# Kernel optimization log

Measured on AMD Instinct MI355X. Metric: run time of the kernel, lower is better.

Reference implementation:

```python
import jax, jax.numpy as jnp
import numpy as np

HIDDEN = 1408
HEADS = 16
HEAD_DIM = 88  # HIDDEN // HEADS
NUM_PATCHES = 576  # (336 // 14) ** 2
SEQ = NUM_PATCHES + 1  # +1 CLS token position in mllama4 rope cache
ROPE_BASE = 10000.0
SCALE = HEAD_DIM ** -0.5


def _rope_cos_sin():
    # Faithful to vLLM Llama4VisionRotaryEmbedding cos/sin cache.
    idx = np.arange(NUM_PATCHES, dtype=np.int64).reshape(NUM_PATCHES, 1)
    idx = np.concatenate([idx, idx[:1]], axis=0)
    idx[-1, -1] = -2  # CLS token id -> zero rotation
    n = int(np.sqrt(NUM_PATCHES))  # patches per side = 24
    fx = idx % n
    fy = idx // n
    rd = HEAD_DIM // 2  # rotary_dim = 44
    inv = 1.0 / ROPE_BASE ** (np.arange(0, rd, 2, dtype=np.float32) / rd)  # (22,)
    # repeat_interleave(2) then cat then [::2] == concat of the two 22-d halves
    freqs = np.concatenate(
        [(fx + 1)[..., None] * inv[None, None, :], (fy + 1)[..., None] * inv[None, None, :]],
        axis=-1,
    )  # (SEQ, 1, 44)
    freqs = np.where(idx.reshape(-1, 1, 1) < 0, 0.0, freqs).astype(np.float32)
    freqs = freqs.squeeze(1)  # (SEQ, 44)
    return jnp.asarray(np.cos(freqs)), jnp.asarray(np.sin(freqs))


_COS, _SIN = _rope_cos_sin()


def _apply_rope(x, cos, sin):
    # x: [B, S, H, D]; complex rotation over adjacent pairs (is_neox_style=False)
    B, S, H, D = x.shape
    xp = x.reshape(B, S, H, D // 2, 2)
    x0, x1 = xp[..., 0], xp[..., 1]
    c = cos[None, :, None, :]  # [1, S, 1, D//2]
    s = sin[None, :, None, :]
    out = jnp.stack([x0 * c - x1 * s, x0 * s + x1 * c], axis=-1)
    return out.reshape(B, S, H, D)


def setup_inputs() -> dict:
    key = jax.random.key(0)
    k1, k2, k3, k4, k5 = jax.random.split(key, 5)
    std = HIDDEN ** -0.5
    return {
        "hidden_states": jax.random.normal(k1, (32, SEQ, HIDDEN), dtype=jnp.float32),
        "w_qkv": jax.random.normal(k2, (HIDDEN, 3 * HIDDEN), dtype=jnp.float32) * std,
        "b_qkv": jax.random.normal(k3, (3 * HIDDEN,), dtype=jnp.float32) * 0.02,
        "w_o": jax.random.normal(k4, (HIDDEN, HIDDEN), dtype=jnp.float32) * std,
        "b_o": jax.random.normal(k5, (HIDDEN,), dtype=jnp.float32) * 0.02,
    }


def reference(hidden_states, w_qkv, b_qkv, w_o, b_o):
    B, S, _ = hidden_states.shape
    qkv = hidden_states @ w_qkv + b_qkv  # [B, S, 3*HIDDEN]
    q, k, v = jnp.split(qkv, 3, axis=-1)
    q = q.reshape(B, S, HEADS, HEAD_DIM)
    k = k.reshape(B, S, HEADS, HEAD_DIM)
    v = v.reshape(B, S, HEADS, HEAD_DIM)
    q = _apply_rope(q, _COS, _SIN)
    k = _apply_rope(k, _COS, _SIN)
    scores = jnp.einsum("bqhd,bkhd->bhqk", q, k) * SCALE
    probs = jax.nn.softmax(scores, axis=-1)
    attn = jnp.einsum("bhqk,bkhd->bqhd", probs, v).reshape(B, S, HIDDEN)
    return attn @ w_o + b_o
```

## Files before the change

### kernel.cpp

```cpp
#include <hip/hip_runtime.h>
#include <math.h>

#define HEADS    16
#define HEAD_DIM 88
#define SEQ      577
#define SEQV     640
#define HIDDEN   1408
#define NQKV     4224
#define NQKV_PAD 4352
#define NOUT_PAD 1536
#define RD       44
#define SCALE_F  0.1066003581778052f
#define MPAD_ROWS 18688
#define NKT      22
#define BUF_SH   32768

typedef __attribute__((ext_vector_type(8))) short bf16x8;
typedef __attribute__((ext_vector_type(4))) float f32x4;

__device__ __forceinline__ unsigned short f2bf(float x) {
    unsigned u = __float_as_uint(x);
    unsigned r = u + 0x7fff + ((u >> 16) & 1);
    return (unsigned short)(r >> 16);
}
__device__ __forceinline__ f32x4 fzero() {
    f32x4 z; z.x = 0.f; z.y = 0.f; z.z = 0.f; z.w = 0.f; return z;
}
__device__ __forceinline__ int xcd_swz(int flat, int nwg) {
    int q = nwg >> 3, r = nwg & 7;
    int x = flat & 7, j = flat >> 3;
    return (x < r ? x * (q + 1) : r * (q + 1) + (x - r) * q) + j;
}

__global__ void rope_precompute(float* __restrict__ cosb, float* __restrict__ sinb) {
    int s = blockIdx.x;
    int j = threadIdx.x;
    if (j >= RD) return;
    float c, sn;
    if (s == SEQ - 1) {
        c = 1.f; sn = 0.f;
    } else {
        int fx = s % 24, fy = s / 24;
        int p = (j < 22) ? j : j - 22;
        float inv = powf(10000.f, -(float)p / 22.f);
        float f = (float)((j < 22 ? fx : fy) + 1) * inv;
        c = cosf(f); sn = sinf(f);
    }
    cosb[s * RD + j] = c;
    sinb[s * RD + j] = sn;
}

__global__ void conv_hs(const float* __restrict__ in, unsigned short* __restrict__ out,
                        long nreal, long ntot) {
    long i = ((long)blockIdx.x * 256 + threadIdx.x) * 4;
    if (i >= ntot) return;
    ushort4 o;
    if (i < nreal) {
        float4 v = *(const float4*)(in + i);
        o = make_ushort4(f2bf(v.x), f2bf(v.y), f2bf(v.z), f2bf(v.w));
    } else {
        o = make_ushort4(0, 0, 0, 0);
    }
    *(ushort4*)(out + i) = o;
}

__global__ void conv_wT(const float* __restrict__ in, unsigned short* __restrict__ out,
                        int R, int Creal) {
    __shared__ float t[32][33];
    int bx = blockIdx.x * 32, by = blockIdx.y * 32;
    int tx = threadIdx.x & 31, ty = threadIdx.x >> 5;
    #pragma unroll
    for (int i = 0; i < 4; ++i) {
        int col = bx + tx;
        t[ty + i * 8][tx] = (col < Creal) ? in[(size_t)(by + ty + i * 8) * Creal + col] : 0.f;
    }
    __syncthreads();
    #pragma unroll
    for (int i = 0; i < 4; ++i)
        out[(size_t)(bx + ty + i * 8) * R + by + tx] = f2bf(t[tx][ty + i * 8]);
}

__device__ __forceinline__ void stage_half(const unsigned short* __restrict__ src,
                                           int kt, unsigned short* lds, int tid) {
    #pragma unroll
    for (int q = 0; q < 2; ++q) {
        int cf = tid + 512 * q;
        int r  = cf >> 3, c = cf & 7;
        int cg = c ^ (r & 7);
        __builtin_amdgcn_global_load_lds(
            (const __attribute__((address_space(1))) void*)(src + (size_t)r * HIDDEN + kt * 64 + cg * 8),
            (__attribute__((address_space(3))) void*)(lds + cf * 8),
            16, 0, 0);
    }
}

template<int N> __device__ __forceinline__ void vwait() {
    if constexpr (N >= 0)
        asm volatile("s_waitcnt vmcnt(%0)" :: "i"(N) : "memory");
}

template<int CBUF, int IH, int JH, bool STG, int SSIDE, int SHALF, int SBUF, int WAITN>
__device__ __forceinline__ void phase8(
    const unsigned short* __restrict__ wsrc, const unsigned short* __restrict__ hsrc,
    unsigned short* smem, int skt, int tid,
    int ww, int wh, int quad, int l15, f32x4 (&acc)[8][4])
{
    bf16x8 afr[4][2], bfr[2][2];
    #pragma unroll
    for (int i2 = 0; i2 < 4; ++i2)
        #pragma unroll
        for (int kk = 0; kk < 2; ++kk) {
            int r = ww * 64 + i2 * 16 + l15;
            afr[i2][kk] = *(const bf16x8*)(smem + CBUF * BUF_SH + IH * 8192
                          + r * 64 + (((kk * 4 + quad) ^ (r & 7)) << 3));
        }
    #pragma unroll
    for (int j2 = 0; j2 < 2; ++j2)
        #pragma unroll
        for (int kk = 0; kk < 2; ++kk) {
            int r = wh * 32 + j2 * 16 + l15;
            bfr[j2][kk] = *(const bf16x8*)(smem + CBUF * BUF_SH + 16384 + JH * 8192
                          + r * 64 + (((kk * 4 + quad) ^ (r & 7)) << 3));
        }
    if constexpr (STG) {
        const unsigned short* s = (SSIDE ? hsrc : wsrc) + (size_t)SHALF * 128 * HIDDEN;
        stage_half(s, skt, smem + SBUF * BUF_SH + (SSIDE ? 16384 : 0) + SHALF * 8192, tid);
    }
    __builtin_amdgcn_sched_barrier(0);
    __builtin_amdgcn_s_barrier();
    __builtin_amdgcn_sched_barrier(0);
    __builtin_amdgcn_s_setprio(1);
    #pragma unroll
    for (int i2 = 0; i2 < 4; ++i2)
        #pragma unroll
        for (int j2 = 0; j2 < 2; ++j2)
            #pragma unroll
            for (int kk = 0; kk < 2; ++kk)
                acc[IH * 4 + i2][JH * 2 + j2] = __builtin_amdgcn_mfma_f32_16x16x32_bf16(
                    afr[i2][kk], bfr[j2][kk], acc[IH * 4 + i2][JH * 2 + j2], 0, 0, 0);
    __builtin_amdgcn_s_setprio(0);
    __builtin_amdgcn_sched_barrier(0);
    vwait<WAITN>();
    __builtin_amdgcn_s_barrier();
    __builtin_amdgcn_sched_barrier(0);
}

__device__ __forceinline__ void gemm256_8ph(
    const unsigned short* __restrict__ wsrc, const unsigned short* __restrict__ hsrc,
    unsigned short* smem, int tid, f32x4 (&acc)[8][4])
{
    const int lane = tid & 63, w8 = tid >> 6;
    const int quad = lane >> 4, l15 = lane & 15;
    const int ww = w8 >> 2, wh = w8 & 3;

    stage_half(wsrc,                0, smem,                  tid);
    stage_half(hsrc,                0, smem + 16384,          tid);
    stage_half(wsrc + 128 * HIDDEN, 0, smem + 8192,           tid);
    stage_half(hsrc + 128 * HIDDEN, 0, smem + 24576,          tid);
    stage_half(wsrc,                1, smem + BUF_SH,         tid);
    stage_half(hsrc,                1, smem + BUF_SH + 16384, tid);
    asm volatile("s_waitcnt vmcnt(4)" ::: "memory");
    __builtin_amdgcn_s_barrier();
    __builtin_amdgcn_sched_barrier(0);

    for (int it = 0; it < 10; ++it) {
        int k1 = 2 * it + 1, k2 = 2 * it + 2, k3 = 2 * it + 3;
        phase8<0,0,0, true,0,1,1,  6>(wsrc, hsrc, smem, k1, tid, ww, wh, quad, l15, acc);
        phase8<0,0,1, true,1,1,1, -1>(wsrc, hsrc, smem, k1, tid, ww, wh, quad, l15, acc);
        phase8<0,1,0, true,0,0,0, -1>(wsrc, hsrc, smem, k2, tid, ww, wh, quad, l15, acc);
        phase8<0,1,1, true,1,0,0,  8>(wsrc, hsrc, smem, k2, tid, ww, wh, quad, l15, acc);
        phase8<1,0,0, true,0,1,0,  6>(wsrc, hsrc, smem, k2, tid, ww, wh, quad, l15, acc);
        phase8<1,0,1, true,1,1,0, -1>(wsrc, hsrc, smem, k2, tid, ww, wh, quad, l15, acc);
        phase8<1,1,0, true,0,0,1, -1>(wsrc, hsrc, smem, k3, tid, ww, wh, quad, l15, acc);
        phase8<1,1,1, true,1,0,1,  8>(wsrc, hsrc, smem, k3, tid, ww, wh, quad, l15, acc);
    }
    phase8<0,0,0, true,0,1,1,  6>(wsrc, hsrc, smem, 21, tid, ww, wh, quad, l15, acc);
    phase8<0,0,1, true,1,1,1, -1>(wsrc, hsrc, smem, 21, tid, ww, wh, quad, l15, acc);
    phase8<0,1,0, false,0,0,0, -1>(wsrc, hsrc, smem, 0, tid, ww, wh, quad, l15, acc);
    phase8<0,1,1, false,0,0,0,  4>(wsrc, hsrc, smem, 0, tid, ww, wh, quad, l15, acc);
    phase8<1,0,0, false,0,0,0,  0>(wsrc, hsrc, smem, 0, tid, ww, wh, quad, l15, acc);
    phase8<1,0,1, false,0,0,0, -1>(wsrc, hsrc, smem, 0, tid, ww, wh, quad, l15, acc);
    phase8<1,1,0, false,0,0,0, -1>(wsrc, hsrc, smem, 0, tid, ww, wh, quad, l15, acc);
    phase8<1,1,1, false,0,0,0, -1>(wsrc, hsrc, smem, 0, tid, ww, wh, quad, l15, acc);
}

__global__ __launch_bounds__(512, 2) void qkv_mfma(
    const unsigned short* __restrict__ hsb, const unsigned short* __restrict__ wt,
    const float* __restrict__ bias, const float* __restrict__ cosb,
    const float* __restrict__ sinb,
    unsigned short* __restrict__ qb, unsigned short* __restrict__ kb,
    unsigned short* __restrict__ vtb,
    int Mchunk, int row_off)
{
    __shared__ unsigned short smem[2 * BUF_SH];
    int tid = threadIdx.x;
    int lane = tid & 63, w8 = tid >> 6;
    int quad = lane >> 4, l15 = lane & 15;
    int ww = w8 >> 2, wh = w8 & 3;

    int nwg  = gridDim.x * gridDim.y;
    int flat = blockIdx.y * gridDim.x + blockIdx.x;
    int wg   = xcd_swz(flat, nwg);
    int n0   = (wg % gridDim.x) * 256;
    int m0   = (wg / gridDim.x) * 256;

    f32x4 acc[8][4];
    #pragma unroll
    for (int i = 0; i < 8; ++i)
        #pragma unroll
        for (int j = 0; j < 4; ++j) acc[i][j] = fzero();

    gemm256_8ph(wt + (size_t)n0 * HIDDEN,
                hsb + (size_t)(row_off + m0) * HIDDEN, smem, tid, acc);

    #pragma unroll
    for (int j = 0; j < 4; ++j) {
        int m = m0 + (j >> 1) * 128 + wh * 32 + (j & 1) * 16 + l15;
        if (m >= Mchunk) continue;
        int bb = m / SEQ;
        int s  = m - bb * SEQ;
        const float* cr = cosb + s * RD;
        const float* sr = sinb + s * RD;
        #pragma unroll
        for (int i = 0; i < 8; ++i) {
            int ng = n0 + (i >> 2) * 128 + ww * 64 + (i & 3) * 16 + quad * 4;
            if (ng >= NQKV) continue;
            int sec = ng / HIDDEN;
            int nn  = ng - sec * HIDDEN;
            int h   = nn / HEAD_DIM;
            int d0  = nn - h * HEAD_DIM;
            int bh  = bb * HEADS + h;
            f32x4 v = acc[i][j];
            const float4 bv = *(const float4*)(bias + ng);
            v.x += bv.x; v.y += bv.y; v.z += bv.z; v.w += bv.w;
            if (sec < 2) {
                int p0 = d0 >> 1;
                float c0 = cr[p0],     s0 = sr[p0];
                float c1 = cr[p0 + 1], s1 = sr[p0 + 1];
                float x0 = v.x, x1 = v.y;
                v.x = x0 * c0 - x1 * s0; v.y = x0 * s0 + x1 * c0;
                x0 = v.z; x1 = v.w;
                v.z = x0 * c1 - x1 * s1; v.w = x0 * s1 + x1 * c1;
                if (sec == 0) { v.x *= SCALE_F; v.y *= SCALE_F; v.z *= SCALE_F; v.w *= SCALE_F; }
                unsigned short* dst = (sec == 0) ? qb : kb;
                ushort4 o = make_ushort4(f2bf(v.x), f2bf(v.y), f2bf(v.z), f2bf(v.w));
                *(ushort4*)(dst + ((size_t)bh * SEQ + s) * HEAD_DIM + d0) = o;
            } else {
                unsigned short* vb = vtb + ((size_t)bh * HEAD_DIM + d0) * SEQV + s;
                vb[0]        = f2bf(v.x);
                vb[SEQV]     = f2bf(v.y);
                vb[2 * SEQV] = f2bf(v.z);
                vb[3 * SEQV] = f2bf(v.w);
            }
        }
    }
}

__global__ __launch_bounds__(512, 2) void out_mfma(
    const unsigned short* __restrict__ ab, const unsigned short* __restrict__ wt,
    const float* __restrict__ bias, float* __restrict__ out,
    int Mchunk, int row_off)
{
    __shared__ unsigned short smem[2 * BUF_SH];
    int tid = threadIdx.x;
    int lane = tid & 63, w8 = tid >> 6;
    int quad = lane >> 4, l15 = lane & 15;
    int ww = w8 >> 2, wh = w8 & 3;

    int nwg  = gridDim.x * gridDim.y;
    int flat = blockIdx.y * gridDim.x + blockIdx.x;
    int wg   = xcd_swz(flat, nwg);
    int n0   = (wg % gridDim.x) * 256;
    int m0   = (wg / gridDim.x) * 256;

    f32x4 acc[8][4];
    #pragma unroll
    for (int i = 0; i < 8; ++i)
        #pragma unroll
        for (int j = 0; j < 4; ++j) acc[i][j] = fzero();

    gemm256_8ph(wt + (size_t)n0 * HIDDEN,
                ab + (size_t)m0 * HIDDEN, smem, tid, acc);

    #pragma unroll
    for (int j = 0; j < 4; ++j) {
        int m = m0 + (j >> 1) * 128 + wh * 32 + (j & 1) * 16 + l15;
        if (m >= Mchunk) continue;
        size_t orow = (size_t)(row_off + m) * HIDDEN;
        #pragma unroll
        for (int i = 0; i < 8; ++i) {
            int nn = n0 + (i >> 2) * 128 + ww * 64 + (i & 3) * 16 + quad * 4;
            if (nn >= HIDDEN) continue;
            f32x4 v = acc[i][j];
            const float4 bv = *(const float4*)(bias + nn);
            v.x += bv.x; v.y += bv.y; v.z += bv.z; v.w += bv.w;
            *(f32x4*)(out + orow + nn) = v;
        }
    }
}

#define QT   128
#define KTT  64
#define KSTR 104
#define VSTR 72
#define PSTR 72
#define RESCALE_THR 8.0f

__global__ __launch_bounds__(256, 3) void attn_mfma(
    const unsigned short* __restrict__ qb, const unsigned short* __restrict__ kb,
    const unsigned short* __restrict__ vtb, unsigned short* __restrict__ awsb)
{
    __shared__ unsigned short Ks[KTT * KSTR];
    __shared__ unsigned short Vt[96 * VSTR];
    __shared__ unsigned short Ps[QT * PSTR];

    int tid = threadIdx.x;
    int lane = tid & 63, wv = tid >> 6;
    int quad = lane >> 4, l15 = lane & 15;

    int nwg  = gridDim.x * gridDim.y * gridDim.z;
    int flat = (blockIdx.z * gridDim.y + blockIdx.y) * gridDim.x + blockIdx.x;
    int w    = xcd_swz(flat, nwg);
    int qblk = w % gridDim.x;
    int rem  = w / gridDim.x;
    int h    = rem % gridDim.y;
    int bb   = rem / gridDim.y;
    int q0   = qblk * QT;
    int bh   = bb * HEADS + h;
    const unsigned short* qg = qb  + (size_t)bh * SEQ * HEAD_DIM;
    const unsigned short* kg = kb  + (size_t)bh * SEQ * HEAD_DIM;
    const unsigned short* vg = vtb + (size_t)bh * HEAD_DIM * SEQV;

    bf16x8 qf[2][3];
    #pragma unroll
    for (int mf = 0; mf < 2; ++mf)
        #pragma unroll
        for (int ks = 0; ks < 3; ++ks)
            qf[mf][ks] = *(const bf16x8*)(qg +
                (size_t)(q0 + wv * 32 + mf * 16 + l15) * HEAD_DIM + ks * 32 + quad * 8);

    f32x4 O[2][6];
    float m_i[2], l_i[2];
    #pragma unroll
    for (int mf = 0; mf < 2; ++mf) {
        #pragma unroll
        for (int nf = 0; nf < 6; ++nf) O[mf][nf] = fzero();
        m_i[mf] = -INFINITY; l_i[mf] = 0.f;
    }

    bf16x8 kr[3], vr[3];
    auto load_tile = [&](int k0) {
        #pragma unroll
        for (int it = 0; it < 3; ++it) {
            int idx = it * 256 + tid;
            int r = idx / 12, c = idx - r * 12;
            bf16x8 v = (bf16x8)(short)0;
            if (c < 11)
                v = *(const bf16x8*)(kg + (size_t)(k0 + r) * HEAD_DIM + c * 8);
            kr[it] = v;
        }
        #pragma unroll
        for (int it = 0; it < 3; ++it) {
            int idx = it * 256 + tid;
            int r = idx >> 3, c = idx & 7;
            vr[it] = *(const bf16x8*)(vg + (size_t)r * SEQV + k0 + c * 8);
        }
    };
    auto write_tile = [&]() {
        #pragma unroll
        for (int it = 0; it < 3; ++it) {
            int idx = it * 256 + tid;
            int r = idx / 12, c = idx - r * 12;
            *(bf16x8*)(Ks + r * KSTR + c * 8) = kr[it];
        }
        #pragma unroll
        for (int it = 0; it < 3; ++it) {
            int idx = it * 256 + tid;
            int r = idx >> 3, c = idx & 7;
            *(bf16x8*)(Vt + r * VSTR + c * 8) = vr[it];
        }
    };

    load_tile(0);
    write_tile();
    __syncthreads();

    for (int k0 = 0; k0 < SEQ; k0 += KTT) {
        int nxt = k0 + KTT;
        if (nxt < SEQ) load_tile(nxt);

        f32x4 sc[2][4];
        #pragma unroll
        for (int mf = 0; mf < 2; ++mf)
            #pragma unroll
            for (int nf = 0; nf < 4; ++nf) sc[mf][nf] = fzero();
        __builtin_amdgcn_s_setprio(1);
        #pragma unroll
        for (int ks = 0; ks < 3; ++ks) {
            #pragma unroll
            for (int nf = 0; nf < 4; ++nf) {
                bf16x8 a = *(const bf16x8*)(Ks + (nf * 16 + l15) * KSTR + ks * 32 + quad * 8);
                sc[0][nf] = __builtin_amdgcn_mfma_f32_16x16x32_bf16(a, qf[0][ks], sc[0][nf], 0, 0, 0);
                sc[1][nf] = __builtin_amdgcn_mfma_f32_16x16x32_bf16(a, qf[1][ks], sc[1][nf], 0, 0, 0);
            }
        }
        __builtin_amdgcn_s_setprio(0);

        #pragma unroll
        for (int mf = 0; mf < 2; ++mf) {
            float pmax = -INFINITY;
            #pragma unroll
            for (int nf = 0; nf < 4; ++nf)
                #pragma unroll
                for (int r = 0; r < 4; ++r)
                    if (k0 + nf * 16 + quad * 4 + r < SEQ)
                        pmax = fmaxf(pmax, sc[mf][nf][r]);
            pmax = fmaxf(pmax, __shfl_xor(pmax, 16));
            pmax = fmaxf(pmax, __shfl_xor(pmax, 32));
            float mold = m_i[mf];
            bool skip = __all(pmax - mold <= RESCALE_THR);
            float mnew = skip ? mold : fmaxf(mold, pmax);
            float rsum = 0.f;
            #pragma unroll
            for (int nf = 0; nf < 4; ++nf) {
                ushort4 o;
                #pragma unroll
                for (int r = 0; r < 4; ++r) {
                    bool valid = (k0 + nf * 16 + quad * 4 + r < SEQ);
                    float p = valid ? __expf(sc[mf][nf][r] - mnew) : 0.f;
                    rsum += p;
                    ((unsigned short*)&o)[r] = f2bf(p);
                }
                *(ushort4*)(Ps + (wv * 32 + mf * 16 + l15) * PSTR + nf * 16 + quad * 4) = o;
            }
            rsum += __shfl_xor(rsum, 16);
            rsum += __shfl_xor(rsum, 32);
            if (!skip) {
                float alpha = __expf(mold - mnew);
                m_i[mf] = mnew;
                l_i[mf] = l_i[mf] * alpha + rsum;
                #pragma unroll
                for (int r = 0; r < 4; ++r) {
                    float ar = __shfl(alpha, quad * 4 + r, 16);
                    #pragma unroll
                    for (int nf = 0; nf < 6; ++nf) O[mf][nf][r] *= ar;
                }
            } else {
                l_i[mf] += rsum;
            }
        }

        __builtin_amdgcn_s_setprio(1);
        #pragma unroll
        for (int ks = 0; ks < 2; ++ks) {
            bf16x8 a0 = *(const bf16x8*)(Ps + (wv * 32 + l15) * PSTR + ks * 32 + quad * 8);
            bf16x8 a1 = *(const bf16x8*)(Ps + (wv * 32 + 16 + l15) * PSTR + ks * 32 + quad * 8);
            #pragma unroll
            for (int nf = 0; nf < 6; ++nf) {
                bf16x8 b = *(const bf16x8*)(Vt + (nf * 16 + l15) * VSTR + ks * 32 + quad * 8);
                O[0][nf] = __builtin_amdgcn_mfma_f32_16x16x32_bf16(a0, b, O[0][nf], 0, 0, 0);
                O[1][nf] = __builtin_amdgcn_mfma_f32_16x16x32_bf16(a1, b, O[1][nf], 0, 0, 0);
            }
        }
        __builtin_amdgcn_s_setprio(0);

        __syncthreads();
        if (nxt < SEQ) {
            write_tile();
            __syncthreads();
        }
    }

    #pragma unroll
    for (int mf = 0; mf < 2; ++mf) {
        #pragma unroll
        for (int r = 0; r < 4; ++r) {
            int row = q0 + wv * 32 + mf * 16 + quad * 4 + r;
            if (row >= SEQ) continue;
            float lb = __shfl(l_i[mf], quad * 4 + r, 16);
            float il = 1.f / lb;
            size_t base = (size_t)(bb * SEQ + row) * HIDDEN + h * HEAD_DIM;
            #pragma unroll
            for (int nf = 0; nf < 6; ++nf) {
                int d = nf * 16 + l15;
                if (d < HEAD_DIM)
                    awsb[base + d] = f2bf(O[mf][nf][r] * il);
            }
        }
    }
}

extern "C" void kernel_launch(void* const* d_in, const int* in_sizes, int n_in,
                              void* d_out, int out_size, void* d_ws, size_t ws_size,
                              hipStream_t stream) {
    const float* hs    = (const float*)d_in[0];
    const float* w_qkv = (const float*)d_in[1];
    const float* b_qkv = (const float*)d_in[2];
    const float* w_o   = (const float*)d_in[3];
    const float* b_o   = (const float*)d_in[4];
    float* out = (float*)d_out;

    char* p = (char*)d_ws;
    auto alloc = [&](size_t bytes) {
        char* r = p; p += (bytes + 255) & ~(size_t)255; return r;
    };
    float*          cosb   = (float*)alloc((size_t)SEQ * RD * 4);
    float*          sinb   = (float*)alloc((size_t)SEQ * RD * 4);
    unsigned short* wqkv_t = (unsigned short*)alloc((size_t)NQKV_PAD * HIDDEN * 2);
    unsigned short* wo_t   = (unsigned short*)alloc((size_t)NOUT_PAD * HIDDEN * 2);
    unsigned short* hs_bf  = (unsigned short*)alloc((size_t)MPAD_ROWS * HIDDEN * 2);
    size_t fixed = (size_t)(p - (char*)d_ws);

    size_t per_batch = 2ull * HEADS * SEQ * HEAD_DIM * 2
                     + (size_t)HEADS * HEAD_DIM * SEQV * 2
                     + (size_t)SEQ * HIDDEN * 2;
    size_t pads = 2ull * 64 * HEAD_DIM * 2 + 16ull * SEQV * 2 + 256ull * HIDDEN * 2 + 16 * 256;
    size_t rem = (ws_size > fixed + pads) ? ws_size - fixed - pads : 0;
    int CB = (int)(rem / per_batch);
    if (CB < 1) CB = 1;
    if (CB > 32) CB = 32;

    unsigned short* qbuf  = (unsigned short*)alloc(((size_t)CB * HEADS * SEQ + 64) * HEAD_DIM * 2);
    unsigned short* kbuf  = (unsigned short*)alloc(((size_t)CB * HEADS * SEQ + 64) * HEAD_DIM * 2);
    unsigned short* vtbuf = (unsigned short*)alloc(((size_t)CB * HEADS * HEAD_DIM + 16) * SEQV * 2);
    unsigned short* awsb  = (unsigned short*)alloc(((size_t)CB * SEQ + 256) * HIDDEN * 2);

    rope_precompute<<<dim3(SEQ), dim3(64), 0, stream>>>(cosb, sinb);

    long nreal = (long)32 * SEQ * HIDDEN;
    long ntot  = (long)MPAD_ROWS * HIDDEN;
    conv_hs<<<dim3((unsigned)((ntot / 4 + 255) / 256)), 256, 0, stream>>>(hs, hs_bf, nreal, ntot);
    conv_wT<<<dim3(NQKV_PAD / 32, HIDDEN / 32), 256, 0, stream>>>(w_qkv, wqkv_t, HIDDEN, NQKV);
    conv_wT<<<dim3(NOUT_PAD / 32, HIDDEN / 32), 256, 0, stream>>>(w_o, wo_t, HIDDEN, HIDDEN);

    for (int b_off = 0; b_off < 32; b_off += CB) {
        int nb = (32 - b_off < CB) ? (32 - b_off) : CB;
        int M = nb * SEQ;

        dim3 g1(NQKV_PAD / 256, (M + 255) / 256);
        qkv_mfma<<<g1, 512, 0, stream>>>(hs_bf, wqkv_t, b_qkv, cosb, sinb,
                                         qbuf, kbuf, vtbuf, M, b_off * SEQ);
        dim3 g2((SEQ + QT - 1) / QT, HEADS, nb);
        attn_mfma<<<g2, 256, 0, stream>>>(qbuf, kbuf, vtbuf, awsb);
        dim3 g3(NOUT_PAD / 256, (M + 255) / 256);
        out_mfma<<<g3, 512, 0, stream>>>(awsb, wo_t, b_o, out, M, b_off * SEQ);
    }
}
```

Measured before the change: 776.8 us.

## Load K and V fragments directly from global memory in attention kernel

Removes the LDS staging of K and V tiles in the attention kernel. Each wave now loads its MFMA operand fragments straight from global memory into registers, and the V loads are placed between the two softmax halves to hide latency. This drops the LDS writes and both __syncthreads per tile, and frees shared memory for occupancy. In exchange, every wave loads the same K/V data redundantly from global memory and cache (4x duplication), register pressure rises, and the workspace padding is enlarged to cover out-of-range fragment reads.

```diff
diff --git a/kernel.cpp b/kernel.cpp
--- a/kernel.cpp
+++ b/kernel.cpp
@@ -301,8 +301,6 @@
 
 #define QT   128
 #define KTT  64
-#define KSTR 104
-#define VSTR 72
 #define PSTR 72
 #define RESCALE_THR 8.0f
 
@@ -310,8 +308,6 @@
     const unsigned short* __restrict__ qb, const unsigned short* __restrict__ kb,
     const unsigned short* __restrict__ vtb, unsigned short* __restrict__ awsb)
 {
-    __shared__ unsigned short Ks[KTT * KSTR];
-    __shared__ unsigned short Vt[96 * VSTR];
     __shared__ unsigned short Ps[QT * PSTR];
 
     int tid = threadIdx.x;
@@ -348,46 +344,17 @@
         m_i[mf] = -INFINITY; l_i[mf] = 0.f;
     }
 
-    bf16x8 kr[3], vr[3];
-    auto load_tile = [&](int k0) {
-        #pragma unroll
-        for (int it = 0; it < 3; ++it) {
-            int idx = it * 256 + tid;
-            int r = idx / 12, c = idx - r * 12;
-            bf16x8 v = (bf16x8)(short)0;
-            if (c < 11)
-                v = *(const bf16x8*)(kg + (size_t)(k0 + r) * HEAD_DIM + c * 8);
-            kr[it] = v;
-        }
-        #pragma unroll
-        for (int it = 0; it < 3; ++it) {
-            int idx = it * 256 + tid;
-            int r = idx >> 3, c = idx & 7;
-            vr[it] = *(const bf16x8*)(vg + (size_t)r * SEQV + k0 + c * 8);
-        }
-    };
-    auto write_tile = [&]() {
-        #pragma unroll
-        for (int it = 0; it < 3; ++it) {
-            int idx = it * 256 + tid;
-            int r = idx / 12, c = idx - r * 12;
-            *(bf16x8*)(Ks + r * KSTR + c * 8) = kr[it];
-        }
-        #pragma unroll
-        for (int it = 0; it < 3; ++it) {
-            int idx = it * 256 + tid;
-            int r = idx >> 3, c = idx & 7;
-            *(bf16x8*)(Vt + r * VSTR + c * 8) = vr[it];
-        }
-    };
-
-    load_tile(0);
-    write_tile();
-    __syncthreads();
-
     for (int k0 = 0; k0 < SEQ; k0 += KTT) {
-        int nxt = k0 + KTT;
-        if (nxt < SEQ) load_tile(nxt);
+        bf16x8 kf[3][4];
+        #pragma unroll
+        for (int ks = 0; ks < 3; ++ks)
+            #pragma unroll
+            for (int nf = 0; nf < 4; ++nf) {
+                bf16x8 v = *(const bf16x8*)(kg +
+                    (size_t)(k0 + nf * 16 + l15) * HEAD_DIM + ks * 32 + quad * 8);
+                if (ks == 2 && quad == 3) v = (bf16x8)(short)0;
+                kf[ks][nf] = v;
+            }
 
         f32x4 sc[2][4];
         #pragma unroll
@@ -399,15 +366,14 @@
         for (int ks = 0; ks < 3; ++ks) {
             #pragma unroll
             for (int nf = 0; nf < 4; ++nf) {
-                bf16x8 a = *(const bf16x8*)(Ks + (nf * 16 + l15) * KSTR + ks * 32 + quad * 8);
-                sc[0][nf] = __builtin_amdgcn_mfma_f32_16x16x32_bf16(a, qf[0][ks], sc[0][nf], 0, 0, 0);
-                sc[1][nf] = __builtin_amdgcn_mfma_f32_16x16x32_bf16(a, qf[1][ks], sc[1][nf], 0, 0, 0);
+                sc[0][nf] = __builtin_amdgcn_mfma_f32_16x16x32_bf16(kf[ks][nf], qf[0][ks], sc[0][nf], 0, 0, 0);
+                sc[1][nf] = __builtin_amdgcn_mfma_f32_16x16x32_bf16(kf[ks][nf], qf[1][ks], sc[1][nf], 0, 0, 0);
             }
         }
         __builtin_amdgcn_s_setprio(0);
 
-        #pragma unroll
-        for (int mf = 0; mf < 2; ++mf) {
+        bf16x8 vf[2][6];
+        auto smx = [&](int mf) {
             float pmax = -INFINITY;
             #pragma unroll
             for (int nf = 0; nf < 4; ++nf)
@@ -448,7 +414,16 @@
             } else {
                 l_i[mf] += rsum;
             }
-        }
+        };
+
+        smx(0);
+        #pragma unroll
+        for (int ks = 0; ks < 2; ++ks)
+            #pragma unroll
+            for (int nf = 0; nf < 6; ++nf)
+                vf[ks][nf] = *(const bf16x8*)(vg +
+                    (size_t)(nf * 16 + l15) * SEQV + k0 + ks * 32 + quad * 8);
+        smx(1);
 
         __builtin_amdgcn_s_setprio(1);
         #pragma unroll
@@ -457,18 +432,11 @@
             bf16x8 a1 = *(const bf16x8*)(Ps + (wv * 32 + 16 + l15) * PSTR + ks * 32 + quad * 8);
             #pragma unroll
             for (int nf = 0; nf < 6; ++nf) {
-                bf16x8 b = *(const bf16x8*)(Vt + (nf * 16 + l15) * VSTR + ks * 32 + quad * 8);
-                O[0][nf] = __builtin_amdgcn_mfma_f32_16x16x32_bf16(a0, b, O[0][nf], 0, 0, 0);
-                O[1][nf] = __builtin_amdgcn_mfma_f32_16x16x32_bf16(a1, b, O[1][nf], 0, 0, 0);
+                O[0][nf] = __builtin_amdgcn_mfma_f32_16x16x32_bf16(a0, vf[ks][nf], O[0][nf], 0, 0, 0);
+                O[1][nf] = __builtin_amdgcn_mfma_f32_16x16x32_bf16(a1, vf[ks][nf], O[1][nf], 0, 0, 0);
             }
         }
         __builtin_amdgcn_s_setprio(0);
-
-        __syncthreads();
-        if (nxt < SEQ) {
-            write_tile();
-            __syncthreads();
-        }
     }
 
     #pragma unroll
@@ -514,15 +482,15 @@
     size_t per_batch = 2ull * HEADS * SEQ * HEAD_DIM * 2
                      + (size_t)HEADS * HEAD_DIM * SEQV * 2
                      + (size_t)SEQ * HIDDEN * 2;
-    size_t pads = 2ull * 64 * HEAD_DIM * 2 + 16ull * SEQV * 2 + 256ull * HIDDEN * 2 + 16 * 256;
+    size_t pads = 2ull * 128 * HEAD_DIM * 2 + 24ull * SEQV * 2 + 256ull * HIDDEN * 2 + 16 * 256;
     size_t rem = (ws_size > fixed + pads) ? ws_size - fixed - pads : 0;
     int CB = (int)(rem / per_batch);
     if (CB < 1) CB = 1;
     if (CB > 32) CB = 32;
 
-    unsigned short* qbuf  = (unsigned short*)alloc(((size_t)CB * HEADS * SEQ + 64) * HEAD_DIM * 2);
-    unsigned short* kbuf  = (unsigned short*)alloc(((size_t)CB * HEADS * SEQ + 64) * HEAD_DIM * 2);
-    unsigned short* vtbuf = (unsigned short*)alloc(((size_t)CB * HEADS * HEAD_DIM + 16) * SEQV * 2);
+    unsigned short* qbuf  = (unsigned short*)alloc(((size_t)CB * HEADS * SEQ + 128) * HEAD_DIM * 2);
+    unsigned short* kbuf  = (unsigned short*)alloc(((size_t)CB * HEADS * SEQ + 128) * HEAD_DIM * 2);
+    unsigned short* vtbuf = (unsigned short*)alloc(((size_t)CB * HEADS * HEAD_DIM + 24) * SEQV * 2);
     unsigned short* awsb  = (unsigned short*)alloc(((size_t)CB * SEQ + 256) * HIDDEN * 2);
 
     rope_precompute<<<dim3(SEQ), dim3(64), 0, stream>>>(cosb, sinb);
```

Result: faster. 759.2 us (-2.3%).
